# Kernel tuning notes

Measured on AMD Instinct MI355X. Metric: run time of the kernel, lower is better.

## Reference

```python
import jax, jax.numpy as jnp
import numpy as np

B, T, C, H = 4, 1024, 1024, 16
D = C // H          # head size 64
CH = 64             # chunk size (min(T,64))
NK = T // CH        # number of key chunks
TOPK = 32           # sparse_topk
SCALE = 1.0 / np.sqrt(D)


def setup_inputs() -> dict:
    key = jax.random.key(0)
    ks = jax.random.split(key, 7)
    x = jax.random.normal(ks[0], (B, T, C), dtype=jnp.float32)
    importance_scores = jax.random.normal(ks[1], (B, T, H), dtype=jnp.float32)
    temperatures = jax.random.uniform(ks[2], (B, H), dtype=jnp.float32)
    Wq = jax.random.normal(ks[3], (C, C), dtype=jnp.float32) * 0.02
    Wk = jax.random.normal(ks[4], (C, C), dtype=jnp.float32) * 0.02
    Wv = jax.random.normal(ks[5], (C, C), dtype=jnp.float32) * 0.02
    Wo = jax.random.normal(ks[6], (C, C), dtype=jnp.float32) * 0.02
    return {"x": x, "importance_scores": importance_scores,
            "temperatures": temperatures, "Wq": Wq, "Wk": Wk, "Wv": Wv, "Wo": Wo}


def reference(x, importance_scores, temperatures, Wq, Wk, Wv, Wo):
    # projections (eval mode: all dropouts are identity)
    q = jnp.nan_to_num(x @ Wq, nan=0.0, posinf=1.0, neginf=-1.0)
    q = q.reshape(B, T, H, D).transpose(0, 2, 1, 3)            # [B,H,T,D]
    k = (x @ Wk).reshape(B, T, H, D).transpose(0, 2, 1, 3)     # [B,H,T,D]
    v = (x @ Wv).reshape(B, T, H, D).transpose(0, 2, 1, 3)
    k_ch = k.reshape(B, H, NK, CH, D)                          # key chunks
    v_ch = v.reshape(B, H, NK, CH, D)

    # scores per (query, key-chunk, in-chunk-key): [B,H,T,NK,CH]
    scores = jnp.einsum('bhqd,bhkcd->bhqkc', q, k_ch) * SCALE
    temp = jnp.clip(temperatures, 0.1, 100.0)[:, :, None, None, None]
    scores = scores / temp

    # sigmoid importance gating (per query position, broadcast over keys)
    imp = jax.nn.sigmoid(importance_scores.transpose(0, 2, 1))  # [B,H,T]
    mask_weight = jax.nn.sigmoid((imp - 0.5) * 10.0)[:, :, :, None, None]
    scores = scores * mask_weight

    # per-chunk top-k filtering (keep scores >= k-th largest, zero the rest)
    top_scores = jax.lax.top_k(scores, TOPK)[0]
    thr = top_scores[..., -1:]
    scores = scores * (scores >= thr).astype(scores.dtype)

    # per-key-chunk softmax (stable, denom clamped), as in the torch loop
    m = jnp.max(scores, axis=-1, keepdims=True)
    e = jnp.exp(scores - m)
    denom = jnp.clip(jnp.sum(e, axis=-1, keepdims=True), 1e-6, None)
    p = e / denom                                               # [B,H,T,NK,CH]

    out = jnp.einsum('bhqkc,bhkcd->bhqd', p, v_ch)              # sum over chunks
    normalizer = jnp.clip(jnp.sum(p, axis=(3, 4)), 1e-6, None)  # [B,H,T]
    out = out / normalizer[..., None]
    out = jnp.nan_to_num(out, nan=0.0, posinf=1.0, neginf=-1.0)

    out = out.transpose(0, 2, 1, 3).reshape(B, T, C)
    return out @ Wo
```

## Files before the change

### kernel.cpp

```cpp
#include <hip/hip_runtime.h>
#include <stdint.h>

typedef _Float16 f16;
typedef _Float16 f16x8 __attribute__((ext_vector_type(8)));
typedef _Float16 f16x4 __attribute__((ext_vector_type(4)));
typedef float f32x4 __attribute__((ext_vector_type(4)));

#define AS1 __attribute__((address_space(1)))
#define AS3 __attribute__((address_space(3)))

#if __has_builtin(__builtin_amdgcn_exp2f)
#define EXP2(x) __builtin_amdgcn_exp2f(x)
#else
#define EXP2(x) exp2f(x)
#endif

__device__ __forceinline__ void gl_lds16(const void* g, void* l) {
  __builtin_amdgcn_global_load_lds((const AS1 uint32_t*)g, (AS3 uint32_t*)l, 16, 0, 0);
}

__device__ __forceinline__ unsigned dpp16sum_u(unsigned v) {
  v += (unsigned)__builtin_amdgcn_update_dpp(0, (int)v, 0x121, 0xf, 0xf, true);
  v += (unsigned)__builtin_amdgcn_update_dpp(0, (int)v, 0x122, 0xf, 0xf, true);
  v += (unsigned)__builtin_amdgcn_update_dpp(0, (int)v, 0x124, 0xf, 0xf, true);
  v += (unsigned)__builtin_amdgcn_update_dpp(0, (int)v, 0x128, 0xf, 0xf, true);
  return v;
}
__device__ __forceinline__ float g16sum_f(float v) {
  v += __builtin_bit_cast(float, __builtin_amdgcn_update_dpp(0, __builtin_bit_cast(int, v), 0x121, 0xf, 0xf, true));
  v += __builtin_bit_cast(float, __builtin_amdgcn_update_dpp(0, __builtin_bit_cast(int, v), 0x122, 0xf, 0xf, true));
  v += __builtin_bit_cast(float, __builtin_amdgcn_update_dpp(0, __builtin_bit_cast(int, v), 0x124, 0xf, 0xf, true));
  v += __builtin_bit_cast(float, __builtin_amdgcn_update_dpp(0, __builtin_bit_cast(int, v), 0x128, 0xf, 0xf, true));
  return v;
}

__global__ void k_prep(const float* __restrict__ x,
                       const float* __restrict__ Wq, const float* __restrict__ Wk,
                       const float* __restrict__ Wv, const float* __restrict__ Wo,
                       f16* __restrict__ xh,
                       f16* __restrict__ Wqt, f16* __restrict__ Wkt,
                       f16* __restrict__ Wvt, f16* __restrict__ Wot) {
  __shared__ __align__(16) f16 lt[64][72];
  const int t = threadIdx.x;
  if (blockIdx.z == 4) {
    int bid2 = blockIdx.y * 16 + blockIdx.x;
    #pragma unroll 4
    for (int it = 0; it < 16; ++it) {
      int i = ((bid2 * 16 + it) * 256 + t) * 4;
      float4 v = *(const float4*)(x + i);
      f16x4 o = { (f16)v.x, (f16)v.y, (f16)v.z, (f16)v.w };
      *(f16x4*)(xh + i) = o;
    }
    return;
  }
  const float* src; f16* dst; float scl;
  switch (blockIdx.z) {
    case 0: src = Wq; dst = Wqt; scl = 1.0f; break;
    case 1: src = Wk; dst = Wkt; scl = 1.0f; break;
    case 2: src = Wv; dst = Wvt; scl = 1.0f; break;
    default: src = Wo; dst = Wot; scl = 0.0625f; break;
  }
  int n0 = blockIdx.x * 64, k0 = blockIdx.y * 64;
  int kk = t >> 4;
  int nn = (t & 15) * 4;
  #pragma unroll
  for (int p = 0; p < 4; ++p) {
    int k = kk + p * 16;
    float4 v = *(const float4*)(src + (size_t)(k0 + k) * 1024 + n0 + nn);
    lt[nn + 0][k] = (f16)(v.x * scl);
    lt[nn + 1][k] = (f16)(v.y * scl);
    lt[nn + 2][k] = (f16)(v.z * scl);
    lt[nn + 3][k] = (f16)(v.w * scl);
  }
  __syncthreads();
  int row = t >> 2;
  int kp = (t & 3) * 16;
  f16* d = dst + (size_t)(n0 + row) * 1024 + k0 + kp;
  *(f16x8*)d       = *(const f16x8*)&lt[row][kp];
  *(f16x8*)(d + 8) = *(const f16x8*)&lt[row][kp + 8];
}

template<int MODE, int TM>
__global__ __launch_bounds__(256, 2)
void k_gemm(const f16* __restrict__ A, const f16* __restrict__ Bt0,
            const f16* __restrict__ A2, const f16* __restrict__ Bt2,
            const f16* __restrict__ Bt1,
            void* __restrict__ out0, void* __restrict__ out1, void* __restrict__ out2) {
  __shared__ __align__(16) f16 As[TM * 64];
  __shared__ __align__(16) f16 Bs[128 * 64];
  __shared__ __align__(16) f16 EP[(MODE == 0) ? 4 * 64 * 72 : 4];
  const int n0 = blockIdx.x * 128, m0 = blockIdx.y * TM;
  const int tid = threadIdx.x, wave = tid >> 6, lane = tid & 63;
  const int l15 = lane & 15, quad = lane >> 4;
  const int wm = (wave >> 1) * (TM / 2), wn = (wave & 1) * 64;
  constexpr int NI = TM / 32;
  constexpr int PA = TM / 32;
  const f16* Bsrc = Bt0;
  int nb = n0;
  if (MODE == 0) {
    if (n0 >= 2048)      { Bsrc = Bt2; nb = n0 - 2048; }
    else if (n0 >= 1024) { Bsrc = Bt1; nb = n0 - 1024; }
  }
  f32x4 acc[NI][4] = {};
  const int sr = lane >> 3, sg = lane & 7;
  const int gl = sg ^ sr;
  const f16* ap[PA];
  const f16* ap2[PA];
  const f16* bp[4];
  #pragma unroll
  for (int p = 0; p < PA; ++p) {
    size_t off = (size_t)(m0 + wave * (TM / 4) + p * 8 + sr) * 1024 + gl * 8;
    ap[p] = A + off;
    if (MODE == 2) ap2[p] = A2 + off;
  }
  #pragma unroll
  for (int p = 0; p < 4; ++p)
    bp[p] = Bsrc + (size_t)(nb + wave * 32 + p * 8 + sr) * 1024 + gl * 8;

  for (int kt = 0; kt < 16; ++kt) {
    __syncthreads();
    #pragma unroll
    for (int p = 0; p < PA; ++p) {
      if (MODE == 2) {
        f16x8 a0 = *(const f16x8*)ap[p];
        f16x8 a1 = *(const f16x8*)ap2[p];
        *(f16x8*)&As[(wave * (TM / 4) + p * 8) * 64 + lane * 8] = a0 + a1;
        ap2[p] += 64;
      } else {
        gl_lds16(ap[p], &As[(wave * (TM / 4) + p * 8) * 64]);
      }
      ap[p] += 64;
    }
    #pragma unroll
    for (int p = 0; p < 4; ++p) {
      gl_lds16(bp[p], &Bs[(wave * 32 + p * 8) * 64]);
      bp[p] += 64;
    }
    __syncthreads();
    #pragma unroll
    for (int ks = 0; ks < 2; ++ks) {
      f16x8 af[NI], bf[4];
      #pragma unroll
      for (int i = 0; i < NI; ++i) {
        int row = wm + i * 16 + l15;
        int g2 = (ks * 4 + quad) ^ (row & 7);
        af[i] = *(const f16x8*)&As[row * 64 + g2 * 8];
      }
      #pragma unroll
      for (int j = 0; j < 4; ++j) {
        int row = wn + j * 16 + l15;
        int g2 = (ks * 4 + quad) ^ (row & 7);
        bf[j] = *(const f16x8*)&Bs[row * 64 + g2 * 8];
      }
      #pragma unroll
      for (int i = 0; i < NI; ++i)
        #pragma unroll
        for (int j = 0; j < 4; ++j)
          acc[i][j] = __builtin_amdgcn_mfma_f32_16x16x32_f16(af[i], bf[j], acc[i][j], 0, 0, 0);
    }
  }

  if (MODE == 0) {
    if (n0 < 2048) {
      f16* ep = &EP[wave * 64 * 72];
      #pragma unroll
      for (int i = 0; i < NI; ++i)
        #pragma unroll
        for (int j = 0; j < 4; ++j)
          #pragma unroll
          for (int r = 0; r < 4; ++r)
            ep[(i * 16 + quad * 4 + r) * 72 + j * 16 + l15] = (f16)acc[i][j][r];
      f16* dst = (n0 < 1024) ? (f16*)out0 : (f16*)out1;
      const int hh = ((n0 + wn) & 1023) >> 6;
      const int r8 = lane >> 3, cg = lane & 7;
      #pragma unroll
      for (int it = 0; it < 8; ++it) {
        int row = it * 8 + r8;
        f16x8 vv = *(const f16x8*)&ep[row * 72 + cg * 8];
        int m = m0 + wm + row;
        int b = m >> 10, t = m & 1023;
        *(f16x8*)&dst[(size_t)((b * 16 + hh) * 1024 + t) * 64 + cg * 8] = vv;
      }
    } else {
      #pragma unroll
      for (int i = 0; i < NI; ++i)
        #pragma unroll
        for (int j = 0; j < 4; ++j) {
          int mb = m0 + wm + i * 16 + quad * 4;
          int b = mb >> 10, t = mb & 1023;
          int n = n0 + wn + j * 16 + l15;
          int nn2 = n & 1023, hh = nn2 >> 6, d = nn2 & 63;
          f16x4 vv = { (f16)acc[i][j][0], (f16)acc[i][j][1], (f16)acc[i][j][2], (f16)acc[i][j][3] };
          *(f16x4*)((f16*)out2 + ((size_t)(b * 16 + hh) * 64 + d) * 1024 + t) = vv;
        }
    }
  } else {
    #pragma unroll
    for (int i = 0; i < NI; ++i)
      #pragma unroll
      for (int j = 0; j < 4; ++j)
        #pragma unroll
        for (int r = 0; r < 4; ++r) {
          int m = m0 + wm + i * 16 + quad * 4 + r;
          int n = n0 + wn + j * 16 + l15;
          ((float*)out0)[(size_t)m * 1024 + n] = acc[i][j][r];
        }
  }
}

__global__ __launch_bounds__(256, 4)
void k_attn(const f16* __restrict__ Q16, const f16* __restrict__ K16, const f16* __restrict__ Vt16,
            const float* __restrict__ imp, const float* __restrict__ temps,
            f16* __restrict__ part0, f16* __restrict__ part1) {
  __shared__ __align__(16) f16 Qs[64 * 64];
  __shared__ __align__(16) f16 Ks[64 * 64];
  __shared__ __align__(16) f16 Vs[64 * 64];
  __shared__ __align__(16) f16 Ps[64 * 64];

  const int bid = blockIdx.x & 1023;
  const int half = blockIdx.x >> 10;
  const int b = bid >> 8, h = (bid >> 4) & 15, qt = bid & 15;
  const int bh = b * 16 + h;
  const int tid = threadIdx.x, wave = tid >> 6, lane = tid & 63;
  const int l15 = lane & 15, quad = lane >> 4;

  float sc = (0.125f * 1.44269504088896340736f) / fminf(fmaxf(temps[bh], 0.1f), 100.0f);
  float rs[4];
  #pragma unroll
  for (int r = 0; r < 4; ++r) {
    int m = wave * 16 + quad * 4 + r;
    int t = qt * 64 + m;
    float is = imp[(size_t)(b * 1024 + t) * 16 + h];
    float s1 = 1.0f / (1.0f + __expf(-is));
    float mwv = 1.0f / (1.0f + __expf(-(s1 - 0.5f) * 10.0f));
    rs[r] = sc * mwv;
  }

  const int sr = lane >> 3, sg = lane & 7;
  const int gls = sg ^ sr;
  const size_t qoff = ((size_t)bh * 1024 + qt * 64) * 64;
  gl_lds16(Q16 + qoff + (size_t)(wave * 16 + sr) * 64 + gls * 8,     &Qs[(wave * 16) * 64]);
  gl_lds16(Q16 + qoff + (size_t)(wave * 16 + 8 + sr) * 64 + gls * 8, &Qs[(wave * 16 + 8) * 64]);

  const size_t kbase = (size_t)bh * 1024 * 64;
  const size_t vbase = (size_t)bh * 64 * 1024;
  const f16* kp0 = K16 + kbase + (size_t)(half * 512 + wave * 16 + sr) * 64 + gls * 8;
  const f16* kp1 = kp0 + 8 * 64;
  const f16* vp0 = Vt16 + vbase + (size_t)(wave * 16 + sr) * 1024 + half * 512 + gls * 8;
  const f16* vp1 = vp0 + 8 * 1024;
  f16* lk0 = &Ks[(wave * 16) * 64];
  f16* lk1 = &Ks[(wave * 16 + 8) * 64];
  f16* lv0 = &Vs[(wave * 16) * 64];
  f16* lv1 = &Vs[(wave * 16 + 8) * 64];

  f32x4 oacc[4] = {};

  for (int ck = 0; ck < 8; ++ck) {
    __syncthreads();
    gl_lds16(kp0, lk0); gl_lds16(kp1, lk1);
    gl_lds16(vp0, lv0); gl_lds16(vp1, lv1);
    kp0 += 4096; kp1 += 4096; vp0 += 64; vp1 += 64;
    __syncthreads();

    f32x4 sacc[4] = {};
    #pragma unroll
    for (int ks = 0; ks < 2; ++ks) {
      int row = wave * 16 + l15;
      int g2 = (ks * 4 + quad) ^ (row & 7);
      f16x8 aq = *(const f16x8*)&Qs[row * 64 + g2 * 8];
      #pragma unroll
      for (int j = 0; j < 4; ++j) {
        int rn = j * 16 + l15;
        int gn = (ks * 4 + quad) ^ (rn & 7);
        f16x8 bk = *(const f16x8*)&Ks[rn * 64 + gn * 8];
        sacc[j] = __builtin_amdgcn_mfma_f32_16x16x32_f16(aq, bk, sacc[j], 0, 0, 0);
      }
    }

    float svc[4][4];
    unsigned key[4][4];
    #pragma unroll
    for (int j = 0; j < 4; ++j)
      #pragma unroll
      for (int r = 0; r < 4; ++r) {
        float xx = __builtin_amdgcn_fmed3f(sacc[j][r] * rs[r], -60.0f, 60.0f);
        svc[j][r] = xx;
        key[j][r] = __builtin_bit_cast(unsigned, xx + 192.0f);
      }

    unsigned tk0 = 0x43000000u, tk1 = 0x43000000u, tk2 = 0x43000000u, tk3 = 0x43000000u;
    #pragma unroll
    for (int bit = 12; bit >= 0; --bit) {
      const unsigned bpv = 1u << (10 + bit);
      unsigned c0 = tk0 | bpv, c1 = tk1 | bpv, c2 = tk2 | bpv, c3 = tk3 | bpv;
      unsigned pk = 0;
      #pragma unroll
      for (int j = 0; j < 4; ++j) {
        pk += (key[j][0] >= c0) ? 1u : 0u;
        pk += (key[j][1] >= c1) ? 0x100u : 0u;
        pk += (key[j][2] >= c2) ? 0x10000u : 0u;
        pk += (key[j][3] >= c3) ? 0x1000000u : 0u;
      }
      pk = dpp16sum_u(pk);
      unsigned ge = ((pk | 0x80808080u) - 0x20202020u) & 0x80808080u;
      tk0 = (ge & 0x80u) ? c0 : tk0;
      tk1 = (ge & 0x8000u) ? c1 : tk1;
      tk2 = (ge & 0x800000u) ? c2 : tk2;
      tk3 = (ge & 0x80000000u) ? c3 : tk3;
    }

    float e[4][4], dinv[4];
    #pragma unroll
    for (int r = 0; r < 4; ++r) {
      const unsigned tkc = (r == 0) ? tk0 : (r == 1) ? tk1 : (r == 2) ? tk2 : tk3;
      #pragma unroll
      for (int j = 0; j < 4; ++j) {
        float xv = (key[j][r] >= tkc) ? svc[j][r] : 0.0f;
        e[j][r] = EXP2(xv);
      }
      float d = (e[0][r] + e[1][r]) + (e[2][r] + e[3][r]);
      d = g16sum_f(d);
      dinv[r] = __builtin_amdgcn_rcpf(d);
    }

    #pragma unroll
    for (int j = 0; j < 4; ++j)
      #pragma unroll
      for (int r = 0; r < 4; ++r) {
        int m = wave * 16 + quad * 4 + r;
        int c = j * 16 + l15;
        int g2 = (c >> 3) ^ (m & 7);
        Ps[m * 64 + g2 * 8 + (c & 7)] = (f16)(e[j][r] * dinv[r]);
      }

    #pragma unroll
    for (int ks = 0; ks < 2; ++ks) {
      int row = wave * 16 + l15;
      int g2 = (ks * 4 + quad) ^ (row & 7);
      f16x8 ap2 = *(const f16x8*)&Ps[row * 64 + g2 * 8];
      #pragma unroll
      for (int j = 0; j < 4; ++j) {
        int rn = j * 16 + l15;
        int gn = (ks * 4 + quad) ^ (rn & 7);
        f16x8 bv = *(const f16x8*)&Vs[rn * 64 + gn * 8];
        oacc[j] = __builtin_amdgcn_mfma_f32_16x16x32_f16(ap2, bv, oacc[j], 0, 0, 0);
      }
    }
  }

  f16* pd = half ? part1 : part0;
  #pragma unroll
  for (int j = 0; j < 4; ++j)
    #pragma unroll
    for (int r = 0; r < 4; ++r) {
      int m = wave * 16 + quad * 4 + r;
      int t = qt * 64 + m;
      int d = j * 16 + l15;
      pd[(size_t)(b * 1024 + t) * 1024 + h * 64 + d] = (f16)oacc[j][r];
    }
}

extern "C" void kernel_launch(void* const* d_in, const int* in_sizes, int n_in,
                              void* d_out, int out_size, void* d_ws, size_t ws_size,
                              hipStream_t stream) {
  (void)in_sizes; (void)n_in; (void)out_size; (void)ws_size;
  const float* x     = (const float*)d_in[0];
  const float* imp   = (const float*)d_in[1];
  const float* temps = (const float*)d_in[2];
  const float* Wq    = (const float*)d_in[3];
  const float* Wk    = (const float*)d_in[4];
  const float* Wv    = (const float*)d_in[5];
  const float* Wo    = (const float*)d_in[6];
  float* out = (float*)d_out;

  char* w = (char*)d_ws;
  f16* xh   = (f16*)w; w += (size_t)4096 * 1024 * 2;
  f16* Wqt  = (f16*)w; w += (size_t)1024 * 1024 * 2;
  f16* Wkt  = (f16*)w; w += (size_t)1024 * 1024 * 2;
  f16* Wvt  = (f16*)w; w += (size_t)1024 * 1024 * 2;
  f16* Wot  = (f16*)w; w += (size_t)1024 * 1024 * 2;
  f16* Q16  = (f16*)w; w += (size_t)4096 * 1024 * 2;
  f16* K16  = (f16*)w; w += (size_t)4096 * 1024 * 2;
  f16* Vt16 = (f16*)w; w += (size_t)4096 * 1024 * 2;
  f16* O16  = (f16*)w; w += (size_t)4096 * 1024 * 2;

  k_prep<<<dim3(16, 16, 5), dim3(256), 0, stream>>>(x, Wq, Wk, Wv, Wo, xh, Wqt, Wkt, Wvt, Wot);
  k_gemm<0, 128><<<dim3(24, 32), dim3(256), 0, stream>>>(xh, Wqt, nullptr, Wvt, Wkt,
                                                         (void*)Q16, (void*)K16, (void*)Vt16);
  k_attn<<<dim3(2048), dim3(256), 0, stream>>>(Q16, K16, Vt16, imp, temps, xh, O16);
  k_gemm<2, 64><<<dim3(8, 64), dim3(256), 0, stream>>>(xh, Wot, O16, nullptr, nullptr,
                                                       (void*)out, nullptr, nullptr);
}
```

Measured before the change: 259.9 us.

## Transpose score MFMA so each lane owns one query row, use permlane reductions

The MFMA operands for QK^T are swapped, so each lane now holds four keys of a single query row instead of four query rows. That lets the radix top-k threshold search use one scalar threshold per lane rather than four byte-packed counters. The cross-lane sums switch from a four-step DPP butterfly to two permlane16/32 swap instructions, the importance gating is computed once per lane, and P is stored with f16x4 vector writes. The main risks are the inline asm using gfx950-specific permlane swaps with manual s_nop hazards, and a changed P layout that must still line up with the PV MFMA.

Result: faster. 245.4 us (-5.6%).

```diff
diff --git a/kernel.cpp b/kernel.cpp
--- a/kernel.cpp
+++ b/kernel.cpp
@@ -19,19 +19,21 @@
   __builtin_amdgcn_global_load_lds((const AS1 uint32_t*)g, (AS3 uint32_t*)l, 16, 0, 0);
 }
 
-__device__ __forceinline__ unsigned dpp16sum_u(unsigned v) {
-  v += (unsigned)__builtin_amdgcn_update_dpp(0, (int)v, 0x121, 0xf, 0xf, true);
-  v += (unsigned)__builtin_amdgcn_update_dpp(0, (int)v, 0x122, 0xf, 0xf, true);
-  v += (unsigned)__builtin_amdgcn_update_dpp(0, (int)v, 0x124, 0xf, 0xf, true);
-  v += (unsigned)__builtin_amdgcn_update_dpp(0, (int)v, 0x128, 0xf, 0xf, true);
-  return v;
-}
-__device__ __forceinline__ float g16sum_f(float v) {
-  v += __builtin_bit_cast(float, __builtin_amdgcn_update_dpp(0, __builtin_bit_cast(int, v), 0x121, 0xf, 0xf, true));
-  v += __builtin_bit_cast(float, __builtin_amdgcn_update_dpp(0, __builtin_bit_cast(int, v), 0x122, 0xf, 0xf, true));
-  v += __builtin_bit_cast(float, __builtin_amdgcn_update_dpp(0, __builtin_bit_cast(int, v), 0x124, 0xf, 0xf, true));
-  v += __builtin_bit_cast(float, __builtin_amdgcn_update_dpp(0, __builtin_bit_cast(int, v), 0x128, 0xf, 0xf, true));
-  return v;
+__device__ __forceinline__ unsigned quadsum_u(unsigned v) {
+  unsigned a = v, b = v;
+  asm("s_nop 1\n\tv_permlane16_swap_b32 %0, %1" : "+v"(a), "+v"(b));
+  unsigned s = a + b;
+  unsigned a2 = s, b2 = s;
+  asm("s_nop 1\n\tv_permlane32_swap_b32 %0, %1" : "+v"(a2), "+v"(b2));
+  return a2 + b2;
+}
+__device__ __forceinline__ float quadsum_f(float v) {
+  float a = v, b = v;
+  asm("s_nop 1\n\tv_permlane16_swap_b32 %0, %1" : "+v"(a), "+v"(b));
+  float s = a + b;
+  float a2 = s, b2 = s;
+  asm("s_nop 1\n\tv_permlane32_swap_b32 %0, %1" : "+v"(a2), "+v"(b2));
+  return a2 + b2;
 }
 
 __global__ void k_prep(const float* __restrict__ x,
@@ -225,16 +227,11 @@
   const int l15 = lane & 15, quad = lane >> 4;
 
   float sc = (0.125f * 1.44269504088896340736f) / fminf(fmaxf(temps[bh], 0.1f), 100.0f);
-  float rs[4];
-  #pragma unroll
-  for (int r = 0; r < 4; ++r) {
-    int m = wave * 16 + quad * 4 + r;
-    int t = qt * 64 + m;
-    float is = imp[(size_t)(b * 1024 + t) * 16 + h];
-    float s1 = 1.0f / (1.0f + __expf(-is));
-    float mwv = 1.0f / (1.0f + __expf(-(s1 - 0.5f) * 10.0f));
-    rs[r] = sc * mwv;
-  }
+  const int tq = qt * 64 + wave * 16 + l15;
+  float is = imp[(size_t)(b * 1024 + tq) * 16 + h];
+  float s1 = 1.0f / (1.0f + __expf(-is));
+  float mwv = 1.0f / (1.0f + __expf(-(s1 - 0.5f) * 10.0f));
+  const float rs = sc * mwv;
 
   const int sr = lane >> 3, sg = lane & 7;
   const int gls = sg ^ sr;
@@ -253,6 +250,12 @@
   f16* lv0 = &Vs[(wave * 16) * 64];
   f16* lv1 = &Vs[(wave * 16 + 8) * 64];
 
+  const int mrow = wave * 16 + l15;
+  f16* pst[4];
+  #pragma unroll
+  for (int j = 0; j < 4; ++j)
+    pst[j] = &Ps[mrow * 64 + (((j * 2 + (quad >> 1)) ^ (l15 & 7)) * 8 + (quad & 1) * 4)];
+
   f32x4 oacc[4] = {};
 
   for (int ck = 0; ck < 8; ++ck) {
@@ -265,73 +268,62 @@
     f32x4 sacc[4] = {};
     #pragma unroll
     for (int ks = 0; ks < 2; ++ks) {
-      int row = wave * 16 + l15;
-      int g2 = (ks * 4 + quad) ^ (row & 7);
-      f16x8 aq = *(const f16x8*)&Qs[row * 64 + g2 * 8];
+      int qr = wave * 16 + l15;
+      int gq = (ks * 4 + quad) ^ (qr & 7);
+      f16x8 bq = *(const f16x8*)&Qs[qr * 64 + gq * 8];
       #pragma unroll
       for (int j = 0; j < 4; ++j) {
-        int rn = j * 16 + l15;
-        int gn = (ks * 4 + quad) ^ (rn & 7);
-        f16x8 bk = *(const f16x8*)&Ks[rn * 64 + gn * 8];
-        sacc[j] = __builtin_amdgcn_mfma_f32_16x16x32_f16(aq, bk, sacc[j], 0, 0, 0);
-      }
-    }
-
-    float svc[4][4];
+        int kr = j * 16 + l15;
+        int gk = (ks * 4 + quad) ^ (kr & 7);
+        f16x8 ak = *(const f16x8*)&Ks[kr * 64 + gk * 8];
+        sacc[j] = __builtin_amdgcn_mfma_f32_16x16x32_f16(ak, bq, sacc[j], 0, 0, 0);
+      }
+    }
+
+    float xx[4][4];
     unsigned key[4][4];
     #pragma unroll
     for (int j = 0; j < 4; ++j)
       #pragma unroll
       for (int r = 0; r < 4; ++r) {
-        float xx = __builtin_amdgcn_fmed3f(sacc[j][r] * rs[r], -60.0f, 60.0f);
-        svc[j][r] = xx;
-        key[j][r] = __builtin_bit_cast(unsigned, xx + 192.0f);
-      }
-
-    unsigned tk0 = 0x43000000u, tk1 = 0x43000000u, tk2 = 0x43000000u, tk3 = 0x43000000u;
+        float v = __builtin_amdgcn_fmed3f(sacc[j][r] * rs, -60.0f, 60.0f) + 192.0f;
+        xx[j][r] = v;
+        key[j][r] = __builtin_bit_cast(unsigned, v);
+      }
+
+    unsigned tk = 0x43000000u;
     #pragma unroll
     for (int bit = 12; bit >= 0; --bit) {
-      const unsigned bpv = 1u << (10 + bit);
-      unsigned c0 = tk0 | bpv, c1 = tk1 | bpv, c2 = tk2 | bpv, c3 = tk3 | bpv;
-      unsigned pk = 0;
-      #pragma unroll
-      for (int j = 0; j < 4; ++j) {
-        pk += (key[j][0] >= c0) ? 1u : 0u;
-        pk += (key[j][1] >= c1) ? 0x100u : 0u;
-        pk += (key[j][2] >= c2) ? 0x10000u : 0u;
-        pk += (key[j][3] >= c3) ? 0x1000000u : 0u;
-      }
-      pk = dpp16sum_u(pk);
-      unsigned ge = ((pk | 0x80808080u) - 0x20202020u) & 0x80808080u;
-      tk0 = (ge & 0x80u) ? c0 : tk0;
-      tk1 = (ge & 0x8000u) ? c1 : tk1;
-      tk2 = (ge & 0x800000u) ? c2 : tk2;
-      tk3 = (ge & 0x80000000u) ? c3 : tk3;
-    }
-
-    float e[4][4], dinv[4];
-    #pragma unroll
-    for (int r = 0; r < 4; ++r) {
-      const unsigned tkc = (r == 0) ? tk0 : (r == 1) ? tk1 : (r == 2) ? tk2 : tk3;
-      #pragma unroll
-      for (int j = 0; j < 4; ++j) {
-        float xv = (key[j][r] >= tkc) ? svc[j][r] : 0.0f;
-        e[j][r] = EXP2(xv);
-      }
-      float d = (e[0][r] + e[1][r]) + (e[2][r] + e[3][r]);
-      d = g16sum_f(d);
-      dinv[r] = __builtin_amdgcn_rcpf(d);
-    }
-
+      const unsigned cand = tk | (1u << (10 + bit));
+      unsigned cq0 = (key[0][0] >= cand) + (key[0][1] >= cand) + (key[0][2] >= cand) + (key[0][3] >= cand);
+      unsigned cq1 = (key[1][0] >= cand) + (key[1][1] >= cand) + (key[1][2] >= cand) + (key[1][3] >= cand);
+      unsigned cq2 = (key[2][0] >= cand) + (key[2][1] >= cand) + (key[2][2] >= cand) + (key[2][3] >= cand);
+      unsigned cq3 = (key[3][0] >= cand) + (key[3][1] >= cand) + (key[3][2] >= cand) + (key[3][3] >= cand);
+      unsigned tot = quadsum_u((cq0 + cq1) + (cq2 + cq3));
+      tk = (tot >= 32u) ? cand : tk;
+    }
+
+    float e[4][4];
     #pragma unroll
     for (int j = 0; j < 4; ++j)
       #pragma unroll
       for (int r = 0; r < 4; ++r) {
-        int m = wave * 16 + quad * 4 + r;
-        int c = j * 16 + l15;
-        int g2 = (c >> 3) ^ (m & 7);
-        Ps[m * 64 + g2 * 8 + (c & 7)] = (f16)(e[j][r] * dinv[r]);
-      }
+        float sel = (key[j][r] >= tk) ? xx[j][r] : 192.0f;
+        e[j][r] = EXP2(sel - 192.0f);
+      }
+    float dsum = ((e[0][0] + e[0][1]) + (e[0][2] + e[0][3]))
+               + ((e[1][0] + e[1][1]) + (e[1][2] + e[1][3]))
+               + ((e[2][0] + e[2][1]) + (e[2][2] + e[2][3]))
+               + ((e[3][0] + e[3][1]) + (e[3][2] + e[3][3]));
+    dsum = quadsum_f(dsum);
+    const float dinv = __builtin_amdgcn_rcpf(dsum);
+
+    #pragma unroll
+    for (int j = 0; j < 4; ++j) {
+      f16x4 pv = { (f16)(e[j][0] * dinv), (f16)(e[j][1] * dinv),
+                   (f16)(e[j][2] * dinv), (f16)(e[j][3] * dinv) };
+      *(f16x4*)pst[j] = pv;
+    }
 
     #pragma unroll
     for (int ks = 0; ks < 2; ++ks) {
```
